# Performance work log

Hardware: AMD Instinct MI355X
Metric: run time of the kernel (lower is better)

## Reference

```python
import jax, jax.numpy as jnp
import numpy as np

BS, N, D, R = 16, 512, 256, 2


def setup_inputs() -> dict:
    key = jax.random.key(0)
    ks = jax.random.split(key, 9)
    s = 1.0 / np.sqrt(D)
    return {
        "encoded_spans": jax.random.normal(ks[0], (BS, N, D), dtype=jnp.float32),
        "w_rel1": jax.random.normal(ks[1], (R, D, D), dtype=jnp.float32) * s,
        "w_root1": jax.random.normal(ks[2], (D, D), dtype=jnp.float32) * s,
        "b1": jnp.zeros((D,), dtype=jnp.float32),
        "w_rel2": jax.random.normal(ks[3], (R, D, D), dtype=jnp.float32) * s,
        "w_root2": jax.random.normal(ks[4], (D, D), dtype=jnp.float32) * s,
        "b2": jnp.zeros((D,), dtype=jnp.float32),
        "aug_adj": jax.random.randint(ks[5], (BS, N, N), 0, 16, dtype=jnp.int64),
        "punct_graph": jax.random.randint(ks[6], (BS, N, N), 0, 16, dtype=jnp.int64),
    }


def reference(encoded_spans, w_rel1, w_root1, b1, w_rel2, w_root2, b2,
              aug_adj, punct_graph):
    # Edge-type masks, exactly as in the torch forward:
    #   type 0: punct edges not in aug graph; type 1: aug edges.
    mask_punct = (punct_graph == 1) & (aug_adj != 1)
    mask_aug = aug_adj == 1
    # masks[r, b, i, j] == 1 means an edge whose message flows x[b,i] -> node j
    # (edge_index = [b*N+i, b*N+j]; PyG aggregates x[src] into edge_index[1]).
    masks = jnp.stack([mask_punct, mask_aug]).astype(encoded_spans.dtype)  # [R,BS,N,N]
    # Per-relation in-degree of each target node (PyG RGCNConv aggr='mean';
    # empty neighborhoods aggregate to 0, i.e. divide by max(deg,1)).
    deg = jnp.maximum(masks.sum(axis=2), 1.0)[..., None]  # [R,BS,N,1]

    def conv(x, w_rel, w_root, b):
        # root/self transform + bias
        out = jnp.einsum('bnd,de->bne', x, w_root) + b
        for r in range(R):
            # mean-aggregate source features into targets, then relation weight
            agg = jnp.einsum('bij,bid->bjd', masks[r], x) / deg[r]
            out = out + jnp.einsum('bjd,de->bje', agg, w_rel[r])
        return out

    # dropout is identity in eval mode
    h = jax.nn.elu(conv(encoded_spans, w_rel1, w_root1, b1))
    h = jax.nn.elu(conv(h, w_rel2, w_root2, b2))
    return h
```

## Files before the change

kernel.cpp:

```cpp
#include <hip/hip_runtime.h>
#include <hip/hip_bf16.h>

#define BS 16
#define NN 512
#define DD 256
#define RR 2
#define M_TOT (BS * NN)
#define KCAT 768

typedef __attribute__((ext_vector_type(8))) short short8;
typedef __attribute__((ext_vector_type(4))) float f32x4;

static __device__ __forceinline__ ushort f2bf(float f) {
  __hip_bfloat16 h = __float2bfloat16(f);
  return *reinterpret_cast<ushort*>(&h);
}

__global__ __launch_bounds__(256) void masks_kernel(
    const int* __restrict__ aug, const int* __restrict__ punct,
    unsigned long long* __restrict__ bitsT) {
  int j = blockIdx.x * 256 + threadIdx.x;
  int w = blockIdx.y;
  int b = blockIdx.z;
  long base = ((long)(b * NN + w * 64)) * NN + j;
  unsigned long long m0 = 0ull, m1 = 0ull;
#pragma unroll 16
  for (int k = 0; k < 64; ++k) {
    int a = aug[base + (long)k * NN];
    int p = punct[base + (long)k * NN];
    unsigned long long isa = (unsigned long long)(a == 1);
    unsigned long long isp = (unsigned long long)((p == 1) & (a != 1));
    m1 |= isa << k;
    m0 |= isp << k;
  }
  bitsT[((0 * BS + b) * NN + j) * 8 + w] = m0;
  bitsT[((1 * BS + b) * NN + j) * 8 + w] = m1;
}

__global__ __launch_bounds__(256) void mt_kernel(
    const unsigned long long* __restrict__ bitsT, ushort* __restrict__ MT,
    float* __restrict__ inv_deg) {
  int j = blockIdx.x, b = blockIdx.y;
  __shared__ unsigned long long words[2][8];
  int t = threadIdx.x;
  if (t < 16)
    words[t >> 3][t & 7] = bitsT[((t >> 3) * BS + b) * NN * 8 + j * 8 + (t & 7)];
  __syncthreads();
  if (t < 2) {
    int s = 0;
#pragma unroll
    for (int w = 0; w < 8; ++w) s += __popcll(words[t][w]);
    if (s < 1) s = 1;
    inv_deg[(t * BS + b) * NN + j] = 1.0f / (float)s;
  }
  int i0 = t * 2;
  int w = i0 >> 6;
#pragma unroll
  for (int r = 0; r < 2; ++r) {
    unsigned long long v = words[r][w] >> (i0 & 63);
    unsigned int packed = ((v & 1) ? 0x3F80u : 0u) | ((v & 2) ? 0x3F800000u : 0u);
    unsigned int* row = reinterpret_cast<unsigned int*>(
        MT + ((size_t)((r * BS + b) * NN + j)) * NN);
    row[t] = packed;
  }
}

__global__ void xprep_kernel(const float* __restrict__ x,
                             ushort* __restrict__ Abig1,
                             ushort* __restrict__ xT) {
  __shared__ float tile[32][33];
  int i0 = blockIdx.x * 32, d0 = blockIdx.y * 32, b = blockIdx.z;
  int tx = threadIdx.x, ty = threadIdx.y;
#pragma unroll
  for (int q = 0; q < 4; ++q) {
    int il = ty + q * 8;
    tile[il][tx] = x[((long)(b * NN + i0 + il)) * DD + d0 + tx];
  }
  __syncthreads();
#pragma unroll
  for (int q = 0; q < 4; ++q) {
    int il = ty + q * 8;
    Abig1[(size_t)(b * NN + i0 + il) * KCAT + d0 + tx] = f2bf(tile[il][tx]);
  }
#pragma unroll
  for (int q = 0; q < 4; ++q) {
    int dl = ty + q * 8;
    xT[((size_t)(b * DD + d0 + dl)) * NN + i0 + tx] = f2bf(tile[tx][dl]);
  }
}

__global__ void transpose_h_kernel(const ushort* __restrict__ A2,
                                   ushort* __restrict__ hT) {
  __shared__ ushort tile[32][33];
  int i0 = blockIdx.x * 32, d0 = blockIdx.y * 32, b = blockIdx.z;
  int tx = threadIdx.x, ty = threadIdx.y;
#pragma unroll
  for (int q = 0; q < 4; ++q) {
    int il = ty + q * 8;
    tile[il][tx] = A2[((long)(b * NN + i0 + il)) * KCAT + d0 + tx];
  }
  __syncthreads();
#pragma unroll
  for (int q = 0; q < 4; ++q) {
    int dl = ty + q * 8;
    hT[((long)(b * DD + d0 + dl)) * NN + i0 + tx] = tile[tx][dl];
  }
}

__global__ void wcat_kernel(const float* __restrict__ wroot1,
                            const float* __restrict__ wrel1,
                            const float* __restrict__ wroot2,
                            const float* __restrict__ wrel2,
                            ushort* __restrict__ W1, ushort* __restrict__ W2) {
  __shared__ float tile[32][33];
  int z = blockIdx.z;
  int layer = z / 3, s = z % 3;
  const float* root = layer ? wroot2 : wroot1;
  const float* rel = layer ? wrel2 : wrel1;
  ushort* dst = layer ? W2 : W1;
  const float* src = (s == 0) ? root : (rel + (size_t)(s - 1) * DD * DD);
  int d0 = blockIdx.x * 32, e0 = blockIdx.y * 32;
  int tx = threadIdx.x, ty = threadIdx.y;
#pragma unroll
  for (int q = 0; q < 4; ++q) {
    int dl = ty + q * 8;
    tile[dl][tx] = src[((long)(d0 + dl)) * DD + e0 + tx];
  }
  __syncthreads();
#pragma unroll
  for (int q = 0; q < 4; ++q) {
    int el = ty + q * 8;
    dst[((size_t)(e0 + el)) * KCAT + s * 256 + d0 + tx] = f2bf(tile[tx][el]);
  }
}

__global__ __launch_bounds__(256) void agg_gemm_kernel(
    const ushort* __restrict__ MT, const ushort* __restrict__ xT,
    const float* __restrict__ inv_deg, ushort* __restrict__ Abig) {
  __shared__ __align__(16) ushort As[2][64][40];
  __shared__ __align__(16) ushort Bs[2][64][40];
  int t = threadIdx.x;
  int rb = blockIdx.z;
  int r = rb >> 4, b = rb & 15;
  int m_base = blockIdx.y * 64;
  int n_base = blockIdx.x * 64;
  int row = t >> 2, col = (t & 3) * 8;
  const ushort* Ag =
      MT + ((size_t)((r * BS + b) * NN + m_base + row)) * NN + col;
  const ushort* Bg = xT + ((size_t)(b * DD + n_base + row)) * NN + col;

  int wave = t >> 6, lane = t & 63;
  int wm = wave >> 1, wn = wave & 1;
  int fr = lane & 15, fq = lane >> 4;

  f32x4 acc[2][2];
#pragma unroll
  for (int i = 0; i < 2; ++i)
#pragma unroll
    for (int jj = 0; jj < 2; ++jj) acc[i][jj] = (f32x4)(0.0f);

  int4 ra = *reinterpret_cast<const int4*>(Ag);
  int4 rbv = *reinterpret_cast<const int4*>(Bg);
  *reinterpret_cast<int4*>(&As[0][row][col]) = ra;
  *reinterpret_cast<int4*>(&Bs[0][row][col]) = rbv;
  int cur = 0;
  __syncthreads();

#pragma unroll 1
  for (int kt = 0; kt < NN / 32; ++kt) {
    int4 na, nb;
    if (kt < NN / 32 - 1) {
      na = *reinterpret_cast<const int4*>(Ag + (kt + 1) * 32);
      nb = *reinterpret_cast<const int4*>(Bg + (kt + 1) * 32);
    }
    short8 a0 = *reinterpret_cast<const short8*>(&As[cur][wm * 32 + fr][fq * 8]);
    short8 a1 = *reinterpret_cast<const short8*>(&As[cur][wm * 32 + 16 + fr][fq * 8]);
    short8 b0 = *reinterpret_cast<const short8*>(&Bs[cur][wn * 32 + fr][fq * 8]);
    short8 b1 = *reinterpret_cast<const short8*>(&Bs[cur][wn * 32 + 16 + fr][fq * 8]);
    acc[0][0] = __builtin_amdgcn_mfma_f32_16x16x32_bf16(a0, b0, acc[0][0], 0, 0, 0);
    acc[0][1] = __builtin_amdgcn_mfma_f32_16x16x32_bf16(a0, b1, acc[0][1], 0, 0, 0);
    acc[1][0] = __builtin_amdgcn_mfma_f32_16x16x32_bf16(a1, b0, acc[1][0], 0, 0, 0);
    acc[1][1] = __builtin_amdgcn_mfma_f32_16x16x32_bf16(a1, b1, acc[1][1], 0, 0, 0);
    if (kt < NN / 32 - 1) {
      *reinterpret_cast<int4*>(&As[cur ^ 1][row][col]) = na;
      *reinterpret_cast<int4*>(&Bs[cur ^ 1][row][col]) = nb;
      __syncthreads();
      cur ^= 1;
    }
  }

  const float* idg = inv_deg + (r * BS + b) * NN + m_base;
#pragma unroll
  for (int mi = 0; mi < 2; ++mi) {
#pragma unroll
    for (int t4 = 0; t4 < 4; ++t4) {
      int jl = wm * 32 + mi * 16 + fq * 4 + t4;
      float idv = idg[jl];
      size_t rowoff =
          (size_t)(b * NN + m_base + jl) * KCAT + 256 + r * 256 + n_base;
#pragma unroll
      for (int ni = 0; ni < 2; ++ni) {
        int d = wn * 32 + ni * 16 + fr;
        Abig[rowoff + d] = f2bf(acc[mi][ni][t4] * idv);
      }
    }
  }
}

template <int MODE>
__global__ __launch_bounds__(256) void main_gemm_kernel(
    const ushort* __restrict__ A, const ushort* __restrict__ WcatT,
    const float* __restrict__ bias, ushort* __restrict__ hOut,
    float* __restrict__ fOut) {
  __shared__ __align__(16) ushort As[2][64][40];
  __shared__ __align__(16) ushort Bs[2][64][40];
  int t = threadIdx.x;
  int m_base = blockIdx.y * 64;
  int n_base = blockIdx.x * 64;
  int row = t >> 2, col = (t & 3) * 8;
  const ushort* Ag = A + (size_t)(m_base + row) * KCAT + col;
  const ushort* Bg = WcatT + (size_t)(n_base + row) * KCAT + col;

  int wave = t >> 6, lane = t & 63;
  int wm = wave >> 1, wn = wave & 1;
  int fr = lane & 15, fq = lane >> 4;

  f32x4 acc[2][2];
#pragma unroll
  for (int i = 0; i < 2; ++i)
#pragma unroll
    for (int jj = 0; jj < 2; ++jj) acc[i][jj] = (f32x4)(0.0f);

  int4 ra = *reinterpret_cast<const int4*>(Ag);
  int4 rbv = *reinterpret_cast<const int4*>(Bg);
  *reinterpret_cast<int4*>(&As[0][row][col]) = ra;
  *reinterpret_cast<int4*>(&Bs[0][row][col]) = rbv;
  int cur = 0;
  __syncthreads();

#pragma unroll 1
  for (int kt = 0; kt < KCAT / 32; ++kt) {
    int4 na, nb;
    if (kt < KCAT / 32 - 1) {
      na = *reinterpret_cast<const int4*>(Ag + (kt + 1) * 32);
      nb = *reinterpret_cast<const int4*>(Bg + (kt + 1) * 32);
    }
    short8 a0 = *reinterpret_cast<const short8*>(&As[cur][wm * 32 + fr][fq * 8]);
    short8 a1 = *reinterpret_cast<const short8*>(&As[cur][wm * 32 + 16 + fr][fq * 8]);
    short8 b0 = *reinterpret_cast<const short8*>(&Bs[cur][wn * 32 + fr][fq * 8]);
    short8 b1 = *reinterpret_cast<const short8*>(&Bs[cur][wn * 32 + 16 + fr][fq * 8]);
    acc[0][0] = __builtin_amdgcn_mfma_f32_16x16x32_bf16(a0, b0, acc[0][0], 0, 0, 0);
    acc[0][1] = __builtin_amdgcn_mfma_f32_16x16x32_bf16(a0, b1, acc[0][1], 0, 0, 0);
    acc[1][0] = __builtin_amdgcn_mfma_f32_16x16x32_bf16(a1, b0, acc[1][0], 0, 0, 0);
    acc[1][1] = __builtin_amdgcn_mfma_f32_16x16x32_bf16(a1, b1, acc[1][1], 0, 0, 0);
    if (kt < KCAT / 32 - 1) {
      *reinterpret_cast<int4*>(&As[cur ^ 1][row][col]) = na;
      *reinterpret_cast<int4*>(&Bs[cur ^ 1][row][col]) = nb;
      __syncthreads();
      cur ^= 1;
    }
  }

#pragma unroll
  for (int mi = 0; mi < 2; ++mi) {
#pragma unroll
    for (int t4 = 0; t4 < 4; ++t4) {
      int m = m_base + wm * 32 + mi * 16 + fq * 4 + t4;
#pragma unroll
      for (int ni = 0; ni < 2; ++ni) {
        int e = n_base + wn * 32 + ni * 16 + fr;
        float v = acc[mi][ni][t4] + bias[e];
        v = v > 0.0f ? v : expm1f(v);
        if (MODE == 0)
          hOut[(size_t)m * KCAT + e] = f2bf(v);
        else
          fOut[(size_t)m * DD + e] = v;
      }
    }
  }
}

extern "C" void kernel_launch(void* const* d_in, const int* in_sizes, int n_in,
                              void* d_out, int out_size, void* d_ws,
                              size_t ws_size, hipStream_t stream) {
  const float* x = (const float*)d_in[0];
  const float* w_rel1 = (const float*)d_in[1];
  const float* w_root1 = (const float*)d_in[2];
  const float* b1 = (const float*)d_in[3];
  const float* w_rel2 = (const float*)d_in[4];
  const float* w_root2 = (const float*)d_in[5];
  const float* b2 = (const float*)d_in[6];
  const int* aug = (const int*)d_in[7];
  const int* punct = (const int*)d_in[8];
  float* out = (float*)d_out;

  char* ws = (char*)d_ws;
  size_t off = 0;
  unsigned long long* bitsT = (unsigned long long*)(ws + off); off += (size_t)RR * BS * NN * 8 * 8;
  float* inv_deg = (float*)(ws + off);                         off += (size_t)RR * BS * NN * 4;
  ushort* MT = (ushort*)(ws + off);                            off += (size_t)RR * BS * NN * NN * 2;
  ushort* xT = (ushort*)(ws + off);                            off += (size_t)BS * DD * NN * 2;
  ushort* WcatT1 = (ushort*)(ws + off);                        off += (size_t)DD * KCAT * 2;
  ushort* WcatT2 = (ushort*)(ws + off);                        off += (size_t)DD * KCAT * 2;
  ushort* Abig1 = (ushort*)(ws + off);                         off += (size_t)M_TOT * KCAT * 2;
  ushort* Abig2 = (ushort*)(ws + off);                         off += (size_t)M_TOT * KCAT * 2;

  masks_kernel<<<dim3(2, 8, 16), 256, 0, stream>>>(aug, punct, bitsT);
  mt_kernel<<<dim3(NN, BS), 256, 0, stream>>>(bitsT, MT, inv_deg);

  xprep_kernel<<<dim3(16, 8, 16), dim3(32, 8), 0, stream>>>(x, Abig1, xT);
  wcat_kernel<<<dim3(8, 8, 6), dim3(32, 8), 0, stream>>>(w_root1, w_rel1,
                                                         w_root2, w_rel2,
                                                         WcatT1, WcatT2);

  agg_gemm_kernel<<<dim3(4, 8, 32), 256, 0, stream>>>(MT, xT, inv_deg, Abig1);
  main_gemm_kernel<0><<<dim3(4, 128), 256, 0, stream>>>(Abig1, WcatT1, b1,
                                                        Abig2, nullptr);

  transpose_h_kernel<<<dim3(16, 8, 16), dim3(32, 8), 0, stream>>>(Abig2, xT);
  agg_gemm_kernel<<<dim3(4, 8, 32), 256, 0, stream>>>(MT, xT, inv_deg, Abig2);
  main_gemm_kernel<1><<<dim3(4, 128), 256, 0, stream>>>(Abig2, WcatT2, b2,
                                                        nullptr, out);
}
```

Before: 171.1 us.

## Enlarge agg GEMM M-tile to 128 and prefetch two k-steps ahead

The aggregation GEMM now computes a 128x64 output tile per block, so each wave holds 4x2 MFMA accumulators and the grid halves along M. This reuses each loaded B tile over twice as many rows. Both GEMMs also keep global loads in registers two k-steps ahead of the LDS double buffer, to hide more load latency. The cost is more registers and LDS per block, fewer blocks for agg (512), and a __syncthreads on every iteration.

```diff
diff --git a/kernel.cpp b/kernel.cpp
--- a/kernel.cpp
+++ b/kernel.cpp
@@ -137,64 +137,80 @@
 __global__ __launch_bounds__(256) void agg_gemm_kernel(
     const ushort* __restrict__ MT, const ushort* __restrict__ xT,
     const float* __restrict__ inv_deg, ushort* __restrict__ Abig) {
-  __shared__ __align__(16) ushort As[2][64][40];
+  __shared__ __align__(16) ushort As[2][128][40];
   __shared__ __align__(16) ushort Bs[2][64][40];
   int t = threadIdx.x;
   int rb = blockIdx.z;
   int r = rb >> 4, b = rb & 15;
-  int m_base = blockIdx.y * 64;
+  int m_base = blockIdx.y * 128;
   int n_base = blockIdx.x * 64;
-  int row = t >> 2, col = (t & 3) * 8;
-  const ushort* Ag =
-      MT + ((size_t)((r * BS + b) * NN + m_base + row)) * NN + col;
-  const ushort* Bg = xT + ((size_t)(b * DD + n_base + row)) * NN + col;
+  int srow = t >> 2, scol = (t & 3) * 8;
+
+  const ushort* Ag0 = MT + ((size_t)((r * BS + b) * NN + m_base + srow)) * NN + scol;
+  const ushort* Ag1 = Ag0 + (size_t)64 * NN;
+  const ushort* Bg = xT + ((size_t)(b * DD + n_base + srow)) * NN + scol;
 
   int wave = t >> 6, lane = t & 63;
   int wm = wave >> 1, wn = wave & 1;
   int fr = lane & 15, fq = lane >> 4;
 
-  f32x4 acc[2][2];
-#pragma unroll
-  for (int i = 0; i < 2; ++i)
+  f32x4 acc[4][2];
+#pragma unroll
+  for (int i = 0; i < 4; ++i)
 #pragma unroll
     for (int jj = 0; jj < 2; ++jj) acc[i][jj] = (f32x4)(0.0f);
 
-  int4 ra = *reinterpret_cast<const int4*>(Ag);
-  int4 rbv = *reinterpret_cast<const int4*>(Bg);
-  *reinterpret_cast<int4*>(&As[0][row][col]) = ra;
-  *reinterpret_cast<int4*>(&Bs[0][row][col]) = rbv;
-  int cur = 0;
-  __syncthreads();
-
-#pragma unroll 1
-  for (int kt = 0; kt < NN / 32; ++kt) {
-    int4 na, nb;
-    if (kt < NN / 32 - 1) {
-      na = *reinterpret_cast<const int4*>(Ag + (kt + 1) * 32);
-      nb = *reinterpret_cast<const int4*>(Bg + (kt + 1) * 32);
-    }
-    short8 a0 = *reinterpret_cast<const short8*>(&As[cur][wm * 32 + fr][fq * 8]);
-    short8 a1 = *reinterpret_cast<const short8*>(&As[cur][wm * 32 + 16 + fr][fq * 8]);
+  const int NT = NN / 32;
+  int4 pa0A, pa1A, pbA, pa0B, pa1B, pbB;
+  pa0A = *reinterpret_cast<const int4*>(Ag0);
+  pa1A = *reinterpret_cast<const int4*>(Ag1);
+  pbA  = *reinterpret_cast<const int4*>(Bg);
+  pa0B = *reinterpret_cast<const int4*>(Ag0 + 32);
+  pa1B = *reinterpret_cast<const int4*>(Ag1 + 32);
+  pbB  = *reinterpret_cast<const int4*>(Bg + 32);
+  *reinterpret_cast<int4*>(&As[0][srow][scol]) = pa0A;
+  *reinterpret_cast<int4*>(&As[0][64 + srow][scol]) = pa1A;
+  *reinterpret_cast<int4*>(&Bs[0][srow][scol]) = pbA;
+  __syncthreads();
+
+#pragma unroll 2
+  for (int kt = 0; kt < NT; ++kt) {
+    if (kt + 2 < NT) {
+      pa0A = *reinterpret_cast<const int4*>(Ag0 + (kt + 2) * 32);
+      pa1A = *reinterpret_cast<const int4*>(Ag1 + (kt + 2) * 32);
+      pbA  = *reinterpret_cast<const int4*>(Bg + (kt + 2) * 32);
+    }
+    int cur = kt & 1;
+    short8 a0 = *reinterpret_cast<const short8*>(&As[cur][wm * 64 + fr][fq * 8]);
+    short8 a1 = *reinterpret_cast<const short8*>(&As[cur][wm * 64 + 16 + fr][fq * 8]);
+    short8 a2 = *reinterpret_cast<const short8*>(&As[cur][wm * 64 + 32 + fr][fq * 8]);
+    short8 a3 = *reinterpret_cast<const short8*>(&As[cur][wm * 64 + 48 + fr][fq * 8]);
     short8 b0 = *reinterpret_cast<const short8*>(&Bs[cur][wn * 32 + fr][fq * 8]);
     short8 b1 = *reinterpret_cast<const short8*>(&Bs[cur][wn * 32 + 16 + fr][fq * 8]);
     acc[0][0] = __builtin_amdgcn_mfma_f32_16x16x32_bf16(a0, b0, acc[0][0], 0, 0, 0);
     acc[0][1] = __builtin_amdgcn_mfma_f32_16x16x32_bf16(a0, b1, acc[0][1], 0, 0, 0);
     acc[1][0] = __builtin_amdgcn_mfma_f32_16x16x32_bf16(a1, b0, acc[1][0], 0, 0, 0);
     acc[1][1] = __builtin_amdgcn_mfma_f32_16x16x32_bf16(a1, b1, acc[1][1], 0, 0, 0);
-    if (kt < NN / 32 - 1) {
-      *reinterpret_cast<int4*>(&As[cur ^ 1][row][col]) = na;
-      *reinterpret_cast<int4*>(&Bs[cur ^ 1][row][col]) = nb;
-      __syncthreads();
-      cur ^= 1;
-    }
+    acc[2][0] = __builtin_amdgcn_mfma_f32_16x16x32_bf16(a2, b0, acc[2][0], 0, 0, 0);
+    acc[2][1] = __builtin_amdgcn_mfma_f32_16x16x32_bf16(a2, b1, acc[2][1], 0, 0, 0);
+    acc[3][0] = __builtin_amdgcn_mfma_f32_16x16x32_bf16(a3, b0, acc[3][0], 0, 0, 0);
+    acc[3][1] = __builtin_amdgcn_mfma_f32_16x16x32_bf16(a3, b1, acc[3][1], 0, 0, 0);
+    if (kt + 1 < NT) {
+      int nxt = cur ^ 1;
+      *reinterpret_cast<int4*>(&As[nxt][srow][scol]) = pa0B;
+      *reinterpret_cast<int4*>(&As[nxt][64 + srow][scol]) = pa1B;
+      *reinterpret_cast<int4*>(&Bs[nxt][srow][scol]) = pbB;
+    }
+    __syncthreads();
+    pa0B = pa0A; pa1B = pa1A; pbB = pbA;
   }
 
   const float* idg = inv_deg + (r * BS + b) * NN + m_base;
 #pragma unroll
-  for (int mi = 0; mi < 2; ++mi) {
+  for (int mi = 0; mi < 4; ++mi) {
 #pragma unroll
     for (int t4 = 0; t4 < 4; ++t4) {
-      int jl = wm * 32 + mi * 16 + fq * 4 + t4;
+      int jl = wm * 64 + mi * 16 + fq * 4 + t4;
       float idv = idg[jl];
       size_t rowoff =
           (size_t)(b * NN + m_base + jl) * KCAT + 256 + r * 256 + n_base;
@@ -217,9 +233,9 @@
   int t = threadIdx.x;
   int m_base = blockIdx.y * 64;
   int n_base = blockIdx.x * 64;
-  int row = t >> 2, col = (t & 3) * 8;
-  const ushort* Ag = A + (size_t)(m_base + row) * KCAT + col;
-  const ushort* Bg = WcatT + (size_t)(n_base + row) * KCAT + col;
+  int srow = t >> 2, scol = (t & 3) * 8;
+  const ushort* Ag = A + (size_t)(m_base + srow) * KCAT + scol;
+  const ushort* Bg = WcatT + (size_t)(n_base + srow) * KCAT + scol;
 
   int wave = t >> 6, lane = t & 63;
   int wm = wave >> 1, wn = wave & 1;
@@ -231,20 +247,23 @@
 #pragma unroll
     for (int jj = 0; jj < 2; ++jj) acc[i][jj] = (f32x4)(0.0f);
 
-  int4 ra = *reinterpret_cast<const int4*>(Ag);
-  int4 rbv = *reinterpret_cast<const int4*>(Bg);
-  *reinterpret_cast<int4*>(&As[0][row][col]) = ra;
-  *reinterpret_cast<int4*>(&Bs[0][row][col]) = rbv;
-  int cur = 0;
-  __syncthreads();
-
-#pragma unroll 1
-  for (int kt = 0; kt < KCAT / 32; ++kt) {
-    int4 na, nb;
-    if (kt < KCAT / 32 - 1) {
-      na = *reinterpret_cast<const int4*>(Ag + (kt + 1) * 32);
-      nb = *reinterpret_cast<const int4*>(Bg + (kt + 1) * 32);
-    }
+  const int NT = KCAT / 32;
+  int4 paA, pbA, paB, pbB;
+  paA = *reinterpret_cast<const int4*>(Ag);
+  pbA = *reinterpret_cast<const int4*>(Bg);
+  paB = *reinterpret_cast<const int4*>(Ag + 32);
+  pbB = *reinterpret_cast<const int4*>(Bg + 32);
+  *reinterpret_cast<int4*>(&As[0][srow][scol]) = paA;
+  *reinterpret_cast<int4*>(&Bs[0][srow][scol]) = pbA;
+  __syncthreads();
+
+#pragma unroll 2
+  for (int kt = 0; kt < NT; ++kt) {
+    if (kt + 2 < NT) {
+      paA = *reinterpret_cast<const int4*>(Ag + (kt + 2) * 32);
+      pbA = *reinterpret_cast<const int4*>(Bg + (kt + 2) * 32);
+    }
+    int cur = kt & 1;
     short8 a0 = *reinterpret_cast<const short8*>(&As[cur][wm * 32 + fr][fq * 8]);
     short8 a1 = *reinterpret_cast<const short8*>(&As[cur][wm * 32 + 16 + fr][fq * 8]);
     short8 b0 = *reinterpret_cast<const short8*>(&Bs[cur][wn * 32 + fr][fq * 8]);
@@ -253,12 +272,13 @@
     acc[0][1] = __builtin_amdgcn_mfma_f32_16x16x32_bf16(a0, b1, acc[0][1], 0, 0, 0);
     acc[1][0] = __builtin_amdgcn_mfma_f32_16x16x32_bf16(a1, b0, acc[1][0], 0, 0, 0);
     acc[1][1] = __builtin_amdgcn_mfma_f32_16x16x32_bf16(a1, b1, acc[1][1], 0, 0, 0);
-    if (kt < KCAT / 32 - 1) {
-      *reinterpret_cast<int4*>(&As[cur ^ 1][row][col]) = na;
-      *reinterpret_cast<int4*>(&Bs[cur ^ 1][row][col]) = nb;
-      __syncthreads();
-      cur ^= 1;
-    }
+    if (kt + 1 < NT) {
+      int nxt = cur ^ 1;
+      *reinterpret_cast<int4*>(&As[nxt][srow][scol]) = paB;
+      *reinterpret_cast<int4*>(&Bs[nxt][srow][scol]) = pbB;
+    }
+    __syncthreads();
+    paB = paA; pbB = pbA;
   }
 
 #pragma unroll
@@ -313,12 +333,12 @@
                                                          w_root2, w_rel2,
                                                          WcatT1, WcatT2);
 
-  agg_gemm_kernel<<<dim3(4, 8, 32), 256, 0, stream>>>(MT, xT, inv_deg, Abig1);
+  agg_gemm_kernel<<<dim3(4, 4, 32), 256, 0, stream>>>(MT, xT, inv_deg, Abig1);
   main_gemm_kernel<0><<<dim3(4, 128), 256, 0, stream>>>(Abig1, WcatT1, b1,
                                                         Abig2, nullptr);
 
   transpose_h_kernel<<<dim3(16, 8, 16), dim3(32, 8), 0, stream>>>(Abig2, xT);
-  agg_gemm_kernel<<<dim3(4, 8, 32), 256, 0, stream>>>(MT, xT, inv_deg, Abig2);
+  agg_gemm_kernel<<<dim3(4, 4, 32), 256, 0, stream>>>(MT, xT, inv_deg, Abig2);
   main_gemm_kernel<1><<<dim3(4, 128), 256, 0, stream>>>(Abig2, WcatT2, b2,
                                                         nullptr, out);
 }
```

Result: slower. 179.3 us (+4.8%).

## Fuse aggregation and weight GEMM into one per-layer kernel

Applied to the files above, without the earlier changes.

Merges the per-relation aggregation GEMM, the concatenated weight GEMM, the bias/ELU epilogue and the transpose for the next layer into a single kernel per layer. The aggregated activations stay in shared memory instead of round-tripping through a large global concat buffer, which removes several launches and a global write/read pass. Operands are now loaded straight from global memory into MFMA fragments without LDS double buffering. The grid shrinks to 256 blocks, so occupancy and latency hiding may suffer.

```diff
diff --git a/kernel.cpp b/kernel.cpp
--- a/kernel.cpp
+++ b/kernel.cpp
@@ -14,6 +14,9 @@
 static __device__ __forceinline__ ushort f2bf(float f) {
   __hip_bfloat16 h = __float2bfloat16(f);
   return *reinterpret_cast<ushort*>(&h);
+}
+static __device__ __forceinline__ uint pack2bf(float a, float b) {
+  return (uint)f2bf(a) | ((uint)f2bf(b) << 16);
 }
 
 __global__ __launch_bounds__(256) void masks_kernel(
@@ -66,7 +69,7 @@
 }
 
 __global__ void xprep_kernel(const float* __restrict__ x,
-                             ushort* __restrict__ Abig1,
+                             ushort* __restrict__ xbf,
                              ushort* __restrict__ xT) {
   __shared__ float tile[32][33];
   int i0 = blockIdx.x * 32, d0 = blockIdx.y * 32, b = blockIdx.z;
@@ -80,30 +83,12 @@
 #pragma unroll
   for (int q = 0; q < 4; ++q) {
     int il = ty + q * 8;
-    Abig1[(size_t)(b * NN + i0 + il) * KCAT + d0 + tx] = f2bf(tile[il][tx]);
+    xbf[(size_t)(b * NN + i0 + il) * DD + d0 + tx] = f2bf(tile[il][tx]);
   }
 #pragma unroll
   for (int q = 0; q < 4; ++q) {
     int dl = ty + q * 8;
     xT[((size_t)(b * DD + d0 + dl)) * NN + i0 + tx] = f2bf(tile[tx][dl]);
-  }
-}
-
-__global__ void transpose_h_kernel(const ushort* __restrict__ A2,
-                                   ushort* __restrict__ hT) {
-  __shared__ ushort tile[32][33];
-  int i0 = blockIdx.x * 32, d0 = blockIdx.y * 32, b = blockIdx.z;
-  int tx = threadIdx.x, ty = threadIdx.y;
-#pragma unroll
-  for (int q = 0; q < 4; ++q) {
-    int il = ty + q * 8;
-    tile[il][tx] = A2[((long)(b * NN + i0 + il)) * KCAT + d0 + tx];
-  }
-  __syncthreads();
-#pragma unroll
-  for (int q = 0; q < 4; ++q) {
-    int dl = ty + q * 8;
-    hT[((long)(b * DD + d0 + dl)) * NN + i0 + tx] = tile[tx][dl];
   }
 }
 
@@ -134,147 +119,184 @@
   }
 }
 
-__global__ __launch_bounds__(256) void agg_gemm_kernel(
-    const ushort* __restrict__ MT, const ushort* __restrict__ xT,
-    const float* __restrict__ inv_deg, ushort* __restrict__ Abig) {
-  __shared__ __align__(16) ushort As[2][64][40];
-  __shared__ __align__(16) ushort Bs[2][64][40];
+template <int LAYER>
+__global__ __launch_bounds__(256) void layer_kernel(
+    const ushort* __restrict__ xbf, const ushort* __restrict__ xT,
+    const ushort* __restrict__ MT, const float* __restrict__ inv_deg,
+    const ushort* __restrict__ WT, const float* __restrict__ bias,
+    ushort* __restrict__ hbf, ushort* __restrict__ hT,
+    float* __restrict__ fOut) {
+  __shared__ __align__(16) char smem[32 * 776 * 2];
+  ushort(*Acat)[776] = reinterpret_cast<ushort(*)[776]>(smem);
+  ushort(*LT)[40] = reinterpret_cast<ushort(*)[40]>(smem);
+
   int t = threadIdx.x;
-  int rb = blockIdx.z;
-  int r = rb >> 4, b = rb & 15;
-  int m_base = blockIdx.y * 64;
-  int n_base = blockIdx.x * 64;
-  int row = t >> 2, col = (t & 3) * 8;
-  const ushort* Ag =
-      MT + ((size_t)((r * BS + b) * NN + m_base + row)) * NN + col;
-  const ushort* Bg = xT + ((size_t)(b * DD + n_base + row)) * NN + col;
-
-  int wave = t >> 6, lane = t & 63;
-  int wm = wave >> 1, wn = wave & 1;
+  int w = t >> 6, lane = t & 63;
   int fr = lane & 15, fq = lane >> 4;
-
-  f32x4 acc[2][2];
-#pragma unroll
-  for (int i = 0; i < 2; ++i)
-#pragma unroll
-    for (int jj = 0; jj < 2; ++jj) acc[i][jj] = (f32x4)(0.0f);
-
-  int4 ra = *reinterpret_cast<const int4*>(Ag);
-  int4 rbv = *reinterpret_cast<const int4*>(Bg);
-  *reinterpret_cast<int4*>(&As[0][row][col]) = ra;
-  *reinterpret_cast<int4*>(&Bs[0][row][col]) = rbv;
-  int cur = 0;
+  int jt = blockIdx.x, b = blockIdx.y;
+  int j0 = jt * 32;
+
+  {
+    int jr = t >> 3, c0 = (t & 7) * 32;
+    const ushort* xr = xbf + (size_t)(b * NN + j0 + jr) * DD + c0;
+#pragma unroll
+    for (int q = 0; q < 4; ++q) {
+      int4 v = *reinterpret_cast<const int4*>(xr + q * 8);
+      *reinterpret_cast<int4*>(&Acat[jr][c0 + q * 8]) = v;
+    }
+  }
+
+  float idv[2][2];
+#pragma unroll
+  for (int r = 0; r < 2; ++r)
+#pragma unroll
+    for (int jf = 0; jf < 2; ++jf)
+      idv[r][jf] = inv_deg[(r * BS + b) * NN + j0 + jf * 16 + fr];
+
+  const ushort* Arow[4];
+#pragma unroll
+  for (int df = 0; df < 4; ++df)
+    Arow[df] = xT + ((size_t)b * DD + w * 64 + df * 16 + fr) * NN + fq * 8;
+  const ushort* Brow[2][2];
+#pragma unroll
+  for (int r = 0; r < 2; ++r)
+#pragma unroll
+    for (int jf = 0; jf < 2; ++jf)
+      Brow[r][jf] =
+          MT + ((size_t)((r * BS + b) * NN) + j0 + jf * 16 + fr) * NN + fq * 8;
+
+  f32x4 accA[2][4][2];
+#pragma unroll
+  for (int r = 0; r < 2; ++r)
+#pragma unroll
+    for (int df = 0; df < 4; ++df)
+#pragma unroll
+      for (int jf = 0; jf < 2; ++jf) accA[r][df][jf] = (f32x4)(0.0f);
+
+#pragma unroll 2
+  for (int kt = 0; kt < NN / 32; ++kt) {
+    int k0 = kt * 32;
+    short8 af[4], bf0[2], bf1[2];
+#pragma unroll
+    for (int df = 0; df < 4; ++df)
+      af[df] = *reinterpret_cast<const short8*>(Arow[df] + k0);
+#pragma unroll
+    for (int jf = 0; jf < 2; ++jf) {
+      bf0[jf] = *reinterpret_cast<const short8*>(Brow[0][jf] + k0);
+      bf1[jf] = *reinterpret_cast<const short8*>(Brow[1][jf] + k0);
+    }
+#pragma unroll
+    for (int df = 0; df < 4; ++df)
+#pragma unroll
+      for (int jf = 0; jf < 2; ++jf) {
+        accA[0][df][jf] = __builtin_amdgcn_mfma_f32_16x16x32_bf16(
+            af[df], bf0[jf], accA[0][df][jf], 0, 0, 0);
+        accA[1][df][jf] = __builtin_amdgcn_mfma_f32_16x16x32_bf16(
+            af[df], bf1[jf], accA[1][df][jf], 0, 0, 0);
+      }
+  }
+
+#pragma unroll
+  for (int r = 0; r < 2; ++r)
+#pragma unroll
+    for (int df = 0; df < 4; ++df)
+#pragma unroll
+      for (int jf = 0; jf < 2; ++jf) {
+        float s = idv[r][jf];
+        uint2 pk;
+        pk.x = pack2bf(accA[r][df][jf][0] * s, accA[r][df][jf][1] * s);
+        pk.y = pack2bf(accA[r][df][jf][2] * s, accA[r][df][jf][3] * s);
+        int row = jf * 16 + fr;
+        int col = 256 + r * 256 + w * 64 + df * 16 + fq * 4;
+        *reinterpret_cast<uint2*>(&Acat[row][col]) = pk;
+      }
   __syncthreads();
 
-#pragma unroll 1
-  for (int kt = 0; kt < NN / 32; ++kt) {
-    int4 na, nb;
-    if (kt < NN / 32 - 1) {
-      na = *reinterpret_cast<const int4*>(Ag + (kt + 1) * 32);
-      nb = *reinterpret_cast<const int4*>(Bg + (kt + 1) * 32);
-    }
-    short8 a0 = *reinterpret_cast<const short8*>(&As[cur][wm * 32 + fr][fq * 8]);
-    short8 a1 = *reinterpret_cast<const short8*>(&As[cur][wm * 32 + 16 + fr][fq * 8]);
-    short8 b0 = *reinterpret_cast<const short8*>(&Bs[cur][wn * 32 + fr][fq * 8]);
-    short8 b1 = *reinterpret_cast<const short8*>(&Bs[cur][wn * 32 + 16 + fr][fq * 8]);
-    acc[0][0] = __builtin_amdgcn_mfma_f32_16x16x32_bf16(a0, b0, acc[0][0], 0, 0, 0);
-    acc[0][1] = __builtin_amdgcn_mfma_f32_16x16x32_bf16(a0, b1, acc[0][1], 0, 0, 0);
-    acc[1][0] = __builtin_amdgcn_mfma_f32_16x16x32_bf16(a1, b0, acc[1][0], 0, 0, 0);
-    acc[1][1] = __builtin_amdgcn_mfma_f32_16x16x32_bf16(a1, b1, acc[1][1], 0, 0, 0);
-    if (kt < NN / 32 - 1) {
-      *reinterpret_cast<int4*>(&As[cur ^ 1][row][col]) = na;
-      *reinterpret_cast<int4*>(&Bs[cur ^ 1][row][col]) = nb;
-      __syncthreads();
-      cur ^= 1;
-    }
-  }
-
-  const float* idg = inv_deg + (r * BS + b) * NN + m_base;
-#pragma unroll
-  for (int mi = 0; mi < 2; ++mi) {
-#pragma unroll
-    for (int t4 = 0; t4 < 4; ++t4) {
-      int jl = wm * 32 + mi * 16 + fq * 4 + t4;
-      float idv = idg[jl];
-      size_t rowoff =
-          (size_t)(b * NN + m_base + jl) * KCAT + 256 + r * 256 + n_base;
-#pragma unroll
-      for (int ni = 0; ni < 2; ++ni) {
-        int d = wn * 32 + ni * 16 + fr;
-        Abig[rowoff + d] = f2bf(acc[mi][ni][t4] * idv);
-      }
-    }
-  }
-}
-
-template <int MODE>
-__global__ __launch_bounds__(256) void main_gemm_kernel(
-    const ushort* __restrict__ A, const ushort* __restrict__ WcatT,
-    const float* __restrict__ bias, ushort* __restrict__ hOut,
-    float* __restrict__ fOut) {
-  __shared__ __align__(16) ushort As[2][64][40];
-  __shared__ __align__(16) ushort Bs[2][64][40];
-  int t = threadIdx.x;
-  int m_base = blockIdx.y * 64;
-  int n_base = blockIdx.x * 64;
-  int row = t >> 2, col = (t & 3) * 8;
-  const ushort* Ag = A + (size_t)(m_base + row) * KCAT + col;
-  const ushort* Bg = WcatT + (size_t)(n_base + row) * KCAT + col;
-
-  int wave = t >> 6, lane = t & 63;
-  int wm = wave >> 1, wn = wave & 1;
-  int fr = lane & 15, fq = lane >> 4;
-
-  f32x4 acc[2][2];
-#pragma unroll
-  for (int i = 0; i < 2; ++i)
-#pragma unroll
-    for (int jj = 0; jj < 2; ++jj) acc[i][jj] = (f32x4)(0.0f);
-
-  int4 ra = *reinterpret_cast<const int4*>(Ag);
-  int4 rbv = *reinterpret_cast<const int4*>(Bg);
-  *reinterpret_cast<int4*>(&As[0][row][col]) = ra;
-  *reinterpret_cast<int4*>(&Bs[0][row][col]) = rbv;
-  int cur = 0;
-  __syncthreads();
-
-#pragma unroll 1
+  const ushort* Wrow[4];
+#pragma unroll
+  for (int ef = 0; ef < 4; ++ef)
+    Wrow[ef] = WT + (size_t)(w * 64 + ef * 16 + fr) * KCAT + fq * 8;
+
+  f32x4 accB[2][4];
+#pragma unroll
+  for (int jf = 0; jf < 2; ++jf)
+#pragma unroll
+    for (int ef = 0; ef < 4; ++ef) accB[jf][ef] = (f32x4)(0.0f);
+
+#pragma unroll 2
   for (int kt = 0; kt < KCAT / 32; ++kt) {
-    int4 na, nb;
-    if (kt < KCAT / 32 - 1) {
-      na = *reinterpret_cast<const int4*>(Ag + (kt + 1) * 32);
-      nb = *reinterpret_cast<const int4*>(Bg + (kt + 1) * 32);
-    }
-    short8 a0 = *reinterpret_cast<const short8*>(&As[cur][wm * 32 + fr][fq * 8]);
-    short8 a1 = *reinterpret_cast<const short8*>(&As[cur][wm * 32 + 16 + fr][fq * 8]);
-    short8 b0 = *reinterpret_cast<const short8*>(&Bs[cur][wn * 32 + fr][fq * 8]);
-    short8 b1 = *reinterpret_cast<const short8*>(&Bs[cur][wn * 32 + 16 + fr][fq * 8]);
-    acc[0][0] = __builtin_amdgcn_mfma_f32_16x16x32_bf16(a0, b0, acc[0][0], 0, 0, 0);
-    acc[0][1] = __builtin_amdgcn_mfma_f32_16x16x32_bf16(a0, b1, acc[0][1], 0, 0, 0);
-    acc[1][0] = __builtin_amdgcn_mfma_f32_16x16x32_bf16(a1, b0, acc[1][0], 0, 0, 0);
-    acc[1][1] = __builtin_amdgcn_mfma_f32_16x16x32_bf16(a1, b1, acc[1][1], 0, 0, 0);
-    if (kt < KCAT / 32 - 1) {
-      *reinterpret_cast<int4*>(&As[cur ^ 1][row][col]) = na;
-      *reinterpret_cast<int4*>(&Bs[cur ^ 1][row][col]) = nb;
-      __syncthreads();
-      cur ^= 1;
-    }
-  }
-
-#pragma unroll
-  for (int mi = 0; mi < 2; ++mi) {
-#pragma unroll
-    for (int t4 = 0; t4 < 4; ++t4) {
-      int m = m_base + wm * 32 + mi * 16 + fq * 4 + t4;
-#pragma unroll
-      for (int ni = 0; ni < 2; ++ni) {
-        int e = n_base + wn * 32 + ni * 16 + fr;
-        float v = acc[mi][ni][t4] + bias[e];
-        v = v > 0.0f ? v : expm1f(v);
-        if (MODE == 0)
-          hOut[(size_t)m * KCAT + e] = f2bf(v);
-        else
+    int k0 = kt * 32;
+    short8 aa[2], bb[4];
+#pragma unroll
+    for (int jf = 0; jf < 2; ++jf)
+      aa[jf] = *reinterpret_cast<const short8*>(&Acat[jf * 16 + fr][k0 + fq * 8]);
+#pragma unroll
+    for (int ef = 0; ef < 4; ++ef)
+      bb[ef] = *reinterpret_cast<const short8*>(Wrow[ef] + k0);
+#pragma unroll
+    for (int jf = 0; jf < 2; ++jf)
+#pragma unroll
+      for (int ef = 0; ef < 4; ++ef)
+        accB[jf][ef] = __builtin_amdgcn_mfma_f32_16x16x32_bf16(
+            aa[jf], bb[ef], accB[jf][ef], 0, 0, 0);
+  }
+
+  float bsv[4];
+#pragma unroll
+  for (int ef = 0; ef < 4; ++ef) bsv[ef] = bias[w * 64 + ef * 16 + fr];
+
+  if (LAYER == 1) {
+#pragma unroll
+    for (int jf = 0; jf < 2; ++jf)
+#pragma unroll
+      for (int ef = 0; ef < 4; ++ef)
+#pragma unroll
+        for (int t4 = 0; t4 < 4; ++t4) {
+          int m = b * NN + j0 + jf * 16 + fq * 4 + t4;
+          int e = w * 64 + ef * 16 + fr;
+          float v = accB[jf][ef][t4] + bsv[ef];
+          v = v > 0.0f ? v : expm1f(v);
           fOut[(size_t)m * DD + e] = v;
+        }
+  } else {
+    uint2 pk[2][4];
+#pragma unroll
+    for (int jf = 0; jf < 2; ++jf)
+#pragma unroll
+      for (int ef = 0; ef < 4; ++ef) {
+        float v0 = accB[jf][ef][0] + bsv[ef];
+        float v1 = accB[jf][ef][1] + bsv[ef];
+        float v2 = accB[jf][ef][2] + bsv[ef];
+        float v3 = accB[jf][ef][3] + bsv[ef];
+        v0 = v0 > 0.0f ? v0 : expm1f(v0);
+        v1 = v1 > 0.0f ? v1 : expm1f(v1);
+        v2 = v2 > 0.0f ? v2 : expm1f(v2);
+        v3 = v3 > 0.0f ? v3 : expm1f(v3);
+        int e = w * 64 + ef * 16 + fr;
+        ushort u0 = f2bf(v0), u1 = f2bf(v1), u2 = f2bf(v2), u3 = f2bf(v3);
+        hbf[(size_t)(b * NN + j0 + jf * 16 + fq * 4 + 0) * DD + e] = u0;
+        hbf[(size_t)(b * NN + j0 + jf * 16 + fq * 4 + 1) * DD + e] = u1;
+        hbf[(size_t)(b * NN + j0 + jf * 16 + fq * 4 + 2) * DD + e] = u2;
+        hbf[(size_t)(b * NN + j0 + jf * 16 + fq * 4 + 3) * DD + e] = u3;
+        pk[jf][ef].x = (uint)u0 | ((uint)u1 << 16);
+        pk[jf][ef].y = (uint)u2 | ((uint)u3 << 16);
+      }
+    __syncthreads();
+#pragma unroll
+    for (int jf = 0; jf < 2; ++jf)
+#pragma unroll
+      for (int ef = 0; ef < 4; ++ef) {
+        int e = w * 64 + ef * 16 + fr;
+        *reinterpret_cast<uint2*>(&LT[e][jf * 16 + fq * 4]) = pk[jf][ef];
+      }
+    __syncthreads();
+    {
+      int e = t;
+      ushort* dst = hT + ((size_t)b * DD + e) * NN + j0;
+#pragma unroll
+      for (int c = 0; c < 4; ++c) {
+        int4 v = *reinterpret_cast<const int4*>(&LT[e][c * 8]);
+        *reinterpret_cast<int4*>(dst + c * 8) = v;
       }
     }
   }
@@ -300,25 +322,21 @@
   float* inv_deg = (float*)(ws + off);                         off += (size_t)RR * BS * NN * 4;
   ushort* MT = (ushort*)(ws + off);                            off += (size_t)RR * BS * NN * NN * 2;
   ushort* xT = (ushort*)(ws + off);                            off += (size_t)BS * DD * NN * 2;
+  ushort* hT = (ushort*)(ws + off);                            off += (size_t)BS * DD * NN * 2;
+  ushort* xbf = (ushort*)(ws + off);                           off += (size_t)M_TOT * DD * 2;
+  ushort* hbf = (ushort*)(ws + off);                           off += (size_t)M_TOT * DD * 2;
   ushort* WcatT1 = (ushort*)(ws + off);                        off += (size_t)DD * KCAT * 2;
   ushort* WcatT2 = (ushort*)(ws + off);                        off += (size_t)DD * KCAT * 2;
-  ushort* Abig1 = (ushort*)(ws + off);                         off += (size_t)M_TOT * KCAT * 2;
-  ushort* Abig2 = (ushort*)(ws + off);                         off += (size_t)M_TOT * KCAT * 2;
 
   masks_kernel<<<dim3(2, 8, 16), 256, 0, stream>>>(aug, punct, bitsT);
   mt_kernel<<<dim3(NN, BS), 256, 0, stream>>>(bitsT, MT, inv_deg);
-
-  xprep_kernel<<<dim3(16, 8, 16), dim3(32, 8), 0, stream>>>(x, Abig1, xT);
+  xprep_kernel<<<dim3(16, 8, 16), dim3(32, 8), 0, stream>>>(x, xbf, xT);
   wcat_kernel<<<dim3(8, 8, 6), dim3(32, 8), 0, stream>>>(w_root1, w_rel1,
                                                          w_root2, w_rel2,
                                                          WcatT1, WcatT2);
 
-  agg_gemm_kernel<<<dim3(4, 8, 32), 256, 0, stream>>>(MT, xT, inv_deg, Abig1);
-  main_gemm_kernel<0><<<dim3(4, 128), 256, 0, stream>>>(Abig1, WcatT1, b1,
-                                                        Abig2, nullptr);
-
-  transpose_h_kernel<<<dim3(16, 8, 16), dim3(32, 8), 0, stream>>>(Abig2, xT);
-  agg_gemm_kernel<<<dim3(4, 8, 32), 256, 0, stream>>>(MT, xT, inv_deg, Abig2);
-  main_gemm_kernel<1><<<dim3(4, 128), 256, 0, stream>>>(Abig2, WcatT2, b2,
-                                                        nullptr, out);
-}
+  layer_kernel<0><<<dim3(16, 16), 256, 0, stream>>>(
+      xbf, xT, MT, inv_deg, WcatT1, b1, hbf, hT, nullptr);
+  layer_kernel<1><<<dim3(16, 16), 256, 0, stream>>>(
+      hbf, hT, MT, inv_deg, WcatT2, b2, nullptr, nullptr, out);
+}
```

After: 176.6 us. +3.2%, slower.
